# Kernel tuning notes

Hardware: AMD Instinct MI355X
Metric: run time of the kernel (lower is better)

## Reference

```python
import jax, jax.numpy as jnp
import numpy as np
import math

# Dimensions (see shape_source)
B, C, NH = 4, 256, 8
VP, VW = 6, 16   # vertical: patches-per-window (outer), windows (inner)
HP, HW = 32, 3   # horizontal: patches-per-window (outer), windows (inner)
NW, P = VW * HW, VP * HP   # 48 windows, 192 patches per window
GRID = 96                   # patch grid is 96x96
SHIFT = (HP // 2, VP // 2)  # (16, 3) = (window_shape[0]//2, window_shape[1]//2)
FF = 4 * C
SCALE = 1.0 / math.sqrt(C)  # source divides by sqrt(embedding_dim), not head_dim


def setup_inputs() -> dict:
    key = jax.random.key(0)
    ks = jax.random.split(key, 17)
    std = 0.02
    n = lambda k, s: (jax.random.normal(k, s, dtype=jnp.float32) * std)
    return {
        "embeddings": jax.random.normal(ks[0], (B, GRID, GRID, C), dtype=jnp.float32),
        "ln1_g": jnp.ones((C,), jnp.float32), "ln1_b": jnp.zeros((C,), jnp.float32),
        "wq": n(ks[1], (C, C)), "bq": jnp.zeros((C,), jnp.float32),
        "wk": n(ks[2], (C, C)), "bk": jnp.zeros((C,), jnp.float32),
        "wv": n(ks[3], (C, C)), "bv": jnp.zeros((C,), jnp.float32),
        "pos_bias": n(ks[4], (NH, P, P)),
        "ln2_g": jnp.ones((C,), jnp.float32), "ln2_b": jnp.zeros((C,), jnp.float32),
        "w1": n(ks[5], (C, FF)), "b1": jnp.zeros((FF,), jnp.float32),
        "w2": n(ks[6], (FF, C)), "b2": jnp.zeros((C,), jnp.float32),
    }


def _ln(x, g, b, eps=1e-5):
    m = jnp.mean(x, axis=-1, keepdims=True)
    v = jnp.mean(jnp.square(x - m), axis=-1, keepdims=True)
    return (x - m) * jax.lax.rsqrt(v + eps) * g + b


def reference(embeddings, ln1_g, ln1_b, wq, bq, wk, bk, wv, bv, pos_bias,
              ln2_g, ln2_b, w1, b1, w2, b2):
    x = jnp.roll(embeddings, SHIFT, axis=(1, 2))
    # part: H=(VP outer, VW inner), W=(HP outer, HW inner) -> [B, NW, P, C]
    p = x.reshape(B, VP, VW, HP, HW, C).transpose(0, 2, 4, 1, 3, 5).reshape(B, NW, P, C)
    y = _ln(p, ln1_g, ln1_b)
    def heads(w, b):
        return (y @ w + b).reshape(B, NW, P, NH, C // NH).transpose(0, 1, 3, 2, 4)
    q, k, v = heads(wq, bq), heads(wk, bk), heads(wv, bv)  # [B, NW, NH, P, Dh]
    logits = jnp.einsum('bwhpd,bwhqd->bwhpq', q, k) * SCALE + pos_bias
    attn = jax.nn.softmax(logits, axis=-1)
    sa = jnp.einsum('bwhpq,bwhqd->bwhpd', attn, v)
    sa = sa.transpose(0, 1, 3, 2, 4).reshape(B, NW, P, C)
    a = p + sa
    h = _ln(a, ln2_g, ln2_b)
    ff = jax.nn.gelu(h @ w1 + b1, approximate=False) @ w2 + b2
    out = a + ff
    # join: inverse of part
    o = out.reshape(B, VW, HW, VP, HP, C).transpose(0, 3, 1, 4, 2, 5).reshape(B, GRID, GRID, C)
    return jnp.roll(o, (-SHIFT[0], -SHIFT[1]), axis=(1, 2))
```

## Files before the change

kernel.cpp:

```cpp
#include <hip/hip_runtime.h>
#include <hip/hip_bf16.h>
#include <cstdint>

using bf16x8 = __attribute__((ext_vector_type(8))) short;
using f32x4  = __attribute__((ext_vector_type(4))) float;
using bf16_t = __hip_bfloat16;

#define DEVI static __device__ __forceinline__

constexpr int kB = 4, kC = 256, kNH = 8, kDh = 32;
constexpr int kVP = 6, kVW = 16, kHP = 32, kHW = 3;
constexpr int kNW = 48, kP = 192, kGRID = 96;
constexpr int kRows = kB * kNW * kP;
constexpr int kFF = 1024;
constexpr float kScale = 0.0625f;

DEVI void row_coords(int row, int& b, int& g1, int& g2) {
  int b_  = row / (kNW * kP);
  int rem = row - b_ * (kNW * kP);
  int w = rem / kP;
  int p = rem - w * kP;
  int vw = w / kHW, hw = w - vw * kHW;
  int vp = p >> 5,  hp = p & 31;
  int r  = vp * kVW + vw;
  int cc = hp * kHW + hw;
  g1 = r + 80;  if (g1 >= kGRID) g1 -= kGRID;
  g2 = cc + 93; if (g2 >= kGRID) g2 -= kGRID;
  b = b_;
}

DEVI float bf2f(short s) {
  union { unsigned u; float f; } c;
  c.u = ((unsigned)(unsigned short)s) << 16;
  return c.f;
}
DEVI short f2bf(float f) {
  bf16_t h = __float2bfloat16(f);
  return *reinterpret_cast<short*>(&h);
}

DEVI void gload16(const void* g, void* l) {
  __builtin_amdgcn_global_load_lds(
      (__attribute__((address_space(1))) void*)(uintptr_t)g,
      (__attribute__((address_space(3))) void*)(uintptr_t)l, 16, 0, 0);
}

DEVI bf16x8 ds_read_b128(uint32_t byte_off) {
  bf16x8 v;
  asm volatile("ds_read_b128 %0, %1" : "=v"(v) : "v"(byte_off));
  return v;
}

DEVI float gelu_fast(float v) {
  const float t2 = v * 1.5957691216f * (1.f + 0.044715f * v * v);
  return v / (1.f + __expf(fminf(-t2, 60.f)));
}

__global__ __launch_bounds__(256) void k_wconv(
    const float* __restrict__ wq, const float* __restrict__ wk,
    const float* __restrict__ wv, const float* __restrict__ w1,
    const float* __restrict__ w2, bf16_t* __restrict__ W) {
  const int i = blockIdx.x * 256 + threadIdx.x;
  if (i < 196608) {
    const int n = i >> 8, k = i & 255;
    const float* src = n < 256 ? wq : (n < 512 ? wk : wv);
    W[i] = __float2bfloat16(src[k * 256 + (n & 255)]);
  } else if (i < 458752) {
    const int j = i - 196608;
    const int n = j >> 8, k = j & 255;
    W[i] = __float2bfloat16(w1[k * 1024 + n]);
  } else if (i < 720896) {
    const int j = i - 458752;
    const int n = j >> 10, k = j & 1023;
    W[i] = __float2bfloat16(w2[k * 256 + n]);
  }
}

__global__ __launch_bounds__(256) void k_ln1(const float* __restrict__ emb,
    const float* __restrict__ gam, const float* __restrict__ bet,
    bf16_t* __restrict__ Y) {
  const int wave = threadIdx.x >> 6, lane = threadIdx.x & 63;
  #pragma unroll
  for (int rr = 0; rr < 2; ++rr) {
    const int row = blockIdx.x * 8 + wave * 2 + rr;
    int b, g1, g2; row_coords(row, b, g1, g2);
    const float* src = emb + (((size_t)b * kGRID + g1) * kGRID + g2) * kC;
    float4 x = *reinterpret_cast<const float4*>(src + lane * 4);
    float s  = x.x + x.y + x.z + x.w;
    float sq = x.x*x.x + x.y*x.y + x.z*x.z + x.w*x.w;
    #pragma unroll
    for (int off = 32; off; off >>= 1) { s += __shfl_xor(s, off); sq += __shfl_xor(sq, off); }
    const float mean = s * (1.f / kC);
    const float rstd = rsqrtf(sq * (1.f / kC) - mean * mean + 1e-5f);
    const float4 g4 = *reinterpret_cast<const float4*>(gam + lane * 4);
    const float4 b4 = *reinterpret_cast<const float4*>(bet + lane * 4);
    short4 o;
    o.x = f2bf((x.x - mean) * rstd * g4.x + b4.x);
    o.y = f2bf((x.y - mean) * rstd * g4.y + b4.y);
    o.z = f2bf((x.z - mean) * rstd * g4.z + b4.z);
    o.w = f2bf((x.w - mean) * rstd * g4.w + b4.w);
    *reinterpret_cast<short4*>(Y + (size_t)row * kC + lane * 4) = o;
  }
}

__global__ __launch_bounds__(256) void k_ln2(const float* __restrict__ emb,
    const bf16_t* __restrict__ SA,
    const float* __restrict__ gam, const float* __restrict__ bet,
    float* __restrict__ A, bf16_t* __restrict__ H) {
  const int wave = threadIdx.x >> 6, lane = threadIdx.x & 63;
  #pragma unroll
  for (int rr = 0; rr < 2; ++rr) {
    const int row = blockIdx.x * 8 + wave * 2 + rr;
    int b, g1, g2; row_coords(row, b, g1, g2);
    const float* src = emb + (((size_t)b * kGRID + g1) * kGRID + g2) * kC;
    float4 x = *reinterpret_cast<const float4*>(src + lane * 4);
    short4 sv = *reinterpret_cast<const short4*>(SA + (size_t)row * kC + lane * 4);
    x.x += bf2f(sv.x); x.y += bf2f(sv.y); x.z += bf2f(sv.z); x.w += bf2f(sv.w);
    *reinterpret_cast<float4*>(A + (size_t)row * kC + lane * 4) = x;
    float s  = x.x + x.y + x.z + x.w;
    float sq = x.x*x.x + x.y*x.y + x.z*x.z + x.w*x.w;
    #pragma unroll
    for (int off = 32; off; off >>= 1) { s += __shfl_xor(s, off); sq += __shfl_xor(sq, off); }
    const float mean = s * (1.f / kC);
    const float rstd = rsqrtf(sq * (1.f / kC) - mean * mean + 1e-5f);
    const float4 g4 = *reinterpret_cast<const float4*>(gam + lane * 4);
    const float4 b4 = *reinterpret_cast<const float4*>(bet + lane * 4);
    short4 o;
    o.x = f2bf((x.x - mean) * rstd * g4.x + b4.x);
    o.y = f2bf((x.y - mean) * rstd * g4.y + b4.y);
    o.z = f2bf((x.z - mean) * rstd * g4.z + b4.z);
    o.w = f2bf((x.w - mean) * rstd * g4.w + b4.w);
    *reinterpret_cast<short4*>(H + (size_t)row * kC + lane * 4) = o;
  }
}

template <int KDIM, int EPI, int GX>
__global__ __launch_bounds__(256, 4) void k_gemm6(
    const bf16_t* __restrict__ Amat, const bf16_t* __restrict__ BT,
    const float* __restrict__ bias0, const float* __restrict__ bias1,
    const float* __restrict__ bias2,
    bf16_t* __restrict__ Obf, const float* __restrict__ Ares,
    float* __restrict__ Out) {
  __shared__ short sm[16384];
  bf16_t* const As0 = (bf16_t*)&sm[0];
  bf16_t* const As1 = (bf16_t*)&sm[4096];
  bf16_t* const Bs0 = (bf16_t*)&sm[8192];
  bf16_t* const Bs1 = (bf16_t*)&sm[12288];
  const int tid = threadIdx.x;
  const int wave = tid >> 6, lane = tid & 63;
  const int lr = lane & 15, kg4 = lane >> 4;
  const int nwg = (kRows / 128) * GX;
  const int wg = (blockIdx.x & 7) * (nwg >> 3) + (blockIdx.x >> 3);
  const int m0 = (wg / GX) * 128, n0 = (wg % GX) * 128;
  const int wm = (wave >> 1) * 64, wn = (wave & 1) * 64;
  const int srow = lane >> 2;
  const int scol = ((lane & 3) ^ (srow & 3)) << 3;

  auto stage = [&](bf16_t* aDst, bf16_t* bDst, int k0) {
    #pragma unroll
    for (int i = 0; i < 2; ++i) {
      const int c = wave * 2 + i;
      const int row = c * 16 + srow;
      gload16(Amat + (size_t)(m0 + row) * KDIM + k0 + scol, aDst + c * 512);
      gload16(BT   + (size_t)(n0 + row) * KDIM + k0 + scol, bDst + c * 512);
    }
  };

  const uint32_t aOff0 = (uint32_t)(uintptr_t)As0;
  const uint32_t aOff1 = (uint32_t)(uintptr_t)As1;
  const uint32_t bOff0 = (uint32_t)(uintptr_t)Bs0;
  const uint32_t bOff1 = (uint32_t)(uintptr_t)Bs1;

  f32x4 acc[4][4] = {};
  auto compute = [&](uint32_t aBase, uint32_t bBase) {
    bf16x8 af[4], bq[4];
    #pragma unroll
    for (int m = 0; m < 4; ++m) {
      const int r = wm + m * 16 + lr;
      af[m] = ds_read_b128(aBase + r * 64 + ((kg4 ^ (r & 3)) << 4));
    }
    #pragma unroll
    for (int n = 0; n < 4; ++n) {
      const int r = wn + n * 16 + lr;
      bq[n] = ds_read_b128(bBase + r * 64 + ((kg4 ^ (r & 3)) << 4));
    }
    asm volatile("s_waitcnt lgkmcnt(0)" ::: "memory");
    __builtin_amdgcn_sched_barrier(0);
    __builtin_amdgcn_s_setprio(1);
    #pragma unroll
    for (int m = 0; m < 4; ++m)
      #pragma unroll
      for (int n = 0; n < 4; ++n)
        acc[m][n] = __builtin_amdgcn_mfma_f32_16x16x32_bf16(af[m], bq[n], acc[m][n], 0, 0, 0);
    __builtin_amdgcn_s_setprio(0);
  };

  stage(As0, Bs0, 0);
  constexpr int NT = KDIM / 32;
  #pragma unroll
  for (int t = 0; t < NT; ++t) {
    if (t + 1 < NT) {
      stage(((t + 1) & 1) ? As1 : As0, ((t + 1) & 1) ? Bs1 : Bs0, (t + 1) * 32);
      asm volatile("s_waitcnt vmcnt(4)" ::: "memory");
    } else {
      asm volatile("s_waitcnt vmcnt(0)" ::: "memory");
    }
    __builtin_amdgcn_sched_barrier(0);
    __builtin_amdgcn_s_barrier();
    compute((t & 1) ? aOff1 : aOff0, (t & 1) ? bOff1 : bOff0);
    __builtin_amdgcn_s_barrier();
  }
  __builtin_amdgcn_sched_barrier(0);

  if constexpr (EPI == 0 || EPI == 1) {
    short* scr = &sm[wave * 4096];
    const int colbase = n0 + wn;
    const float* bp;
    int cb;
    if constexpr (EPI == 0) {
      const int which = colbase >> 8;
      bp = which == 0 ? bias0 : (which == 1 ? bias1 : bias2);
      cb = colbase & 255;
    } else { bp = bias0; cb = colbase; }
    #pragma unroll
    for (int m = 0; m < 4; ++m)
      #pragma unroll
      for (int n = 0; n < 4; ++n)
        #pragma unroll
        for (int r = 0; r < 4; ++r) {
          const int lrow = m * 16 + kg4 * 4 + r;
          const int lcol = n * 16 + lr;
          float v = acc[m][n][r] + bp[cb + lcol];
          if constexpr (EPI == 1) v = gelu_fast(v);
          const int sc = lcol ^ ((lrow & 3) << 4);
          scr[lrow * 64 + sc] = f2bf(v);
        }
    const int rl = lane >> 3, cl = (lane & 7) * 8;
    bf16_t* const obase = (EPI == 0)
        ? Obf + (size_t)(colbase >> 8) * kRows * kC
        : Obf;
    const int ld = (EPI == 0) ? kC : kFF;
    #pragma unroll
    for (int p = 0; p < 8; ++p) {
      const int lrow = p * 8 + rl;
      const int sc = cl ^ ((lrow & 3) << 4);
      bf16x8 v = *reinterpret_cast<const bf16x8*>(&scr[lrow * 64 + sc]);
      *reinterpret_cast<bf16x8*>(
          obase + (size_t)(m0 + wm + lrow) * ld + cb + cl) = v;
    }
  } else {
    float* scrf = reinterpret_cast<float*>(&sm[wave * 4096]);
    #pragma unroll
    for (int h = 0; h < 2; ++h) {
      #pragma unroll
      for (int m = 0; m < 4; ++m)
        #pragma unroll
        for (int nn = 0; nn < 2; ++nn) {
          const int n = h * 2 + nn;
          #pragma unroll
          for (int r = 0; r < 4; ++r) {
            const int lrow = m * 16 + kg4 * 4 + r;
            const int lcol = nn * 16 + lr;
            scrf[lrow * 32 + (lcol ^ ((lrow & 3) << 3))] =
                acc[m][n][r] + bias0[n0 + wn + n * 16 + lr];
          }
        }
      const int rl = lane >> 3, cl = (lane & 7) * 4;
      #pragma unroll
      for (int p = 0; p < 8; ++p) {
        const int lrow = p * 8 + rl;
        const int row = m0 + wm + lrow;
        const int col = n0 + wn + h * 32 + cl;
        float4 v = *reinterpret_cast<const float4*>(
            &scrf[lrow * 32 + (cl ^ ((lrow & 3) << 3))]);
        const float4 a4 = *reinterpret_cast<const float4*>(
            &Ares[(size_t)row * kC + col]);
        v.x += a4.x; v.y += a4.y; v.z += a4.z; v.w += a4.w;
        int b, g1, g2; row_coords(row, b, g1, g2);
        *reinterpret_cast<float4*>(
            &Out[(((size_t)b * kGRID + g1) * kGRID + g2) * kC + col]) = v;
      }
      if (h == 0) __builtin_amdgcn_s_barrier();
    }
  }
}

constexpr int kKsPad = 40;
constexpr int kVtPad = 200;
constexpr int kPlPad = 200;
__global__ __launch_bounds__(256) void k_attn(
    const bf16_t* __restrict__ Q, const bf16_t* __restrict__ K,
    const bf16_t* __restrict__ V, const float* __restrict__ pos,
    bf16_t* __restrict__ SA) {
  __shared__ short Ks[kP * kKsPad];
  __shared__ short Vt[kDh * kVtPad];
  __shared__ short Pl[4 * 16 * kPlPad];
  const int bw = blockIdx.x >> 3, h = blockIdx.x & 7;
  const int rowbase = bw * kP, colbase = h * kDh;
  const int tid = threadIdx.x, wave = tid >> 6, lane = tid & 63;
  const int lr = lane & 15, kg = lane >> 4;
  const int wq0 = wave * 48;
  const float* pb = pos + (size_t)h * kP * kP;

  #pragma unroll
  for (int i = 0; i < 3; ++i) {
    const int c = tid + i * 256;
    const int row = c >> 2, dch = (c & 3) * 8;
    const size_t gbase = (size_t)(rowbase + row) * kC + colbase + dch;
    bf16x8 kv = *reinterpret_cast<const bf16x8*>(K + gbase);
    *reinterpret_cast<bf16x8*>(&Ks[row * kKsPad + dch]) = kv;
    bf16x8 vv = *reinterpret_cast<const bf16x8*>(V + gbase);
    #pragma unroll
    for (int e = 0; e < 8; ++e) Vt[(dch + e) * kVtPad + row] = vv[e];
  }
  __syncthreads();

  for (int m = 0; m < 3; ++m) {
    const int rbase = wq0 + m * 16;
    bf16x8 aq = *reinterpret_cast<const bf16x8*>(
        Q + (size_t)(rowbase + rbase + lr) * kC + colbase + kg * 8);
    f32x4 s[12];
    #pragma unroll
    for (int n = 0; n < 12; ++n) {
      bf16x8 bk = *reinterpret_cast<const bf16x8*>(&Ks[(n * 16 + lr) * kKsPad + kg * 8]);
      s[n] = __builtin_amdgcn_mfma_f32_16x16x32_bf16(aq, bk, (f32x4){0.f, 0.f, 0.f, 0.f}, 0, 0, 0);
    }
    float mx[4] = {-1e30f, -1e30f, -1e30f, -1e30f};
    #pragma unroll
    for (int n = 0; n < 12; ++n) {
      #pragma unroll
      for (int r = 0; r < 4; ++r) {
        const float lg = fmaf(s[n][r], kScale,
                              pb[(size_t)(rbase + kg * 4 + r) * kP + n * 16 + lr]);
        s[n][r] = lg;
        mx[r] = fmaxf(mx[r], lg);
      }
    }
    #pragma unroll
    for (int r = 0; r < 4; ++r)
      #pragma unroll
      for (int off = 8; off; off >>= 1) mx[r] = fmaxf(mx[r], __shfl_xor(mx[r], off));
    float sm4[4] = {0.f, 0.f, 0.f, 0.f};
    #pragma unroll
    for (int n = 0; n < 12; ++n)
      #pragma unroll
      for (int r = 0; r < 4; ++r) {
        const float e = __expf(s[n][r] - mx[r]);
        s[n][r] = e;
        sm4[r] += e;
      }
    #pragma unroll
    for (int r = 0; r < 4; ++r) {
      #pragma unroll
      for (int off = 8; off; off >>= 1) sm4[r] += __shfl_xor(sm4[r], off);
      sm4[r] = 1.f / sm4[r];
    }
    #pragma unroll
    for (int n = 0; n < 12; ++n)
      #pragma unroll
      for (int r = 0; r < 4; ++r)
        Pl[(wave * 16 + kg * 4 + r) * kPlPad + n * 16 + lr] = f2bf(s[n][r] * sm4[r]);
    f32x4 o0 = {0.f, 0.f, 0.f, 0.f}, o1 = {0.f, 0.f, 0.f, 0.f};
    #pragma unroll
    for (int kk = 0; kk < 6; ++kk) {
      bf16x8 ap = *reinterpret_cast<const bf16x8*>(&Pl[(wave * 16 + lr) * kPlPad + kk * 32 + kg * 8]);
      bf16x8 b0 = *reinterpret_cast<const bf16x8*>(&Vt[lr * kVtPad + kk * 32 + kg * 8]);
      bf16x8 b1 = *reinterpret_cast<const bf16x8*>(&Vt[(16 + lr) * kVtPad + kk * 32 + kg * 8]);
      o0 = __builtin_amdgcn_mfma_f32_16x16x32_bf16(ap, b0, o0, 0, 0, 0);
      o1 = __builtin_amdgcn_mfma_f32_16x16x32_bf16(ap, b1, o1, 0, 0, 0);
    }
    short* scr2 = &Pl[wave * 16 * kPlPad];
    #pragma unroll
    for (int r = 0; r < 4; ++r) {
      scr2[(kg * 4 + r) * 32 + lr]      = f2bf(o0[r]);
      scr2[(kg * 4 + r) * 32 + 16 + lr] = f2bf(o1[r]);
    }
    {
      const int rrow = lane >> 2, c0 = (lane & 3) * 8;
      bf16x8 v = *reinterpret_cast<const bf16x8*>(&scr2[rrow * 32 + c0]);
      *reinterpret_cast<bf16x8*>(
          SA + (size_t)(rowbase + rbase + rrow) * kC + colbase + c0) = v;
    }
  }
}

extern "C" void kernel_launch(void* const* d_in, const int* in_sizes, int n_in,
                              void* d_out, int out_size, void* d_ws, size_t ws_size,
                              hipStream_t stream) {
  const float* emb  = (const float*)d_in[0];
  const float* ln1g = (const float*)d_in[1];
  const float* ln1b = (const float*)d_in[2];
  const float* wq   = (const float*)d_in[3];
  const float* bq   = (const float*)d_in[4];
  const float* wk   = (const float*)d_in[5];
  const float* bk   = (const float*)d_in[6];
  const float* wv   = (const float*)d_in[7];
  const float* bv   = (const float*)d_in[8];
  const float* pos  = (const float*)d_in[9];
  const float* ln2g = (const float*)d_in[10];
  const float* ln2b = (const float*)d_in[11];
  const float* w1   = (const float*)d_in[12];
  const float* b1   = (const float*)d_in[13];
  const float* w2   = (const float*)d_in[14];
  const float* b2   = (const float*)d_in[15];

  char* ws = (char*)d_ws;
  const size_t nYb = (size_t)kRows * kC * 2;
  bf16_t* Y    = (bf16_t*)(ws);
  bf16_t* Qb   = (bf16_t*)(ws + nYb);
  bf16_t* SAb  = (bf16_t*)(ws + nYb * 4);
  float*  Abuf = (float*) (ws + nYb * 5);
  bf16_t* H    = (bf16_t*)(ws + nYb * 5 + (size_t)kRows * kC * 4);
  bf16_t* G    = (bf16_t*)(ws);
  bf16_t* W    = (bf16_t*)(ws + nYb * 5 + (size_t)kRows * kC * 4 + nYb);
  bf16_t* WqkvT = W;
  bf16_t* W1T   = W + 768 * 256;
  bf16_t* W2T   = W1T + 1024 * 256;

  k_wconv<<<2816, 256, 0, stream>>>(wq, wk, wv, w1, w2, W);
  k_ln1<<<kRows / 8, 256, 0, stream>>>(emb, ln1g, ln1b, Y);
  k_gemm6<256, 0, 6><<<(kRows / 128) * 6, 256, 0, stream>>>(
      Y, WqkvT, bq, bk, bv, Qb, nullptr, nullptr);
  k_attn<<<kB * kNW * kNH, 256, 0, stream>>>(
      Qb, Qb + (size_t)kRows * kC, Qb + 2 * (size_t)kRows * kC, pos, SAb);
  k_ln2<<<kRows / 8, 256, 0, stream>>>(emb, SAb, ln2g, ln2b, Abuf, H);
  k_gemm6<256, 1, 8><<<(kRows / 128) * 8, 256, 0, stream>>>(
      H, W1T, b1, nullptr, nullptr, G, nullptr, nullptr);
  k_gemm6<1024, 2, 2><<<(kRows / 128) * 2, 256, 0, stream>>>(
      G, W2T, b2, nullptr, nullptr, nullptr, Abuf, (float*)d_out);
}
```

Before: 177.3 us.

## Enlarge GEMM tiles to 256x256 with 512-thread workgroups

Replaces the 128x128, 4-wave GEMM with a 256x256 tile computed by 8 waves. Each wave now owns a 128x64 sub-tile, and the LDS double buffers are doubled in size. The aim is more operand reuse per global load and fewer workgroups. The epilogues are restructured to drain the larger accumulator through per-wave scratch in chunks, with a new swizzle. The cost is far fewer blocks: only 144 for the FFN down-projection, which may leave many CUs idle and cut latency hiding at one workgroup per CU.

```diff
diff --git a/kernel.cpp b/kernel.cpp
--- a/kernel.cpp
+++ b/kernel.cpp
@@ -135,24 +135,24 @@
 }
 
 template <int KDIM, int EPI, int GX>
-__global__ __launch_bounds__(256, 4) void k_gemm6(
+__global__ __launch_bounds__(512, 1) void k_gemm7(
     const bf16_t* __restrict__ Amat, const bf16_t* __restrict__ BT,
     const float* __restrict__ bias0, const float* __restrict__ bias1,
     const float* __restrict__ bias2,
     bf16_t* __restrict__ Obf, const float* __restrict__ Ares,
     float* __restrict__ Out) {
-  __shared__ short sm[16384];
+  __shared__ short sm[32768];
   bf16_t* const As0 = (bf16_t*)&sm[0];
-  bf16_t* const As1 = (bf16_t*)&sm[4096];
-  bf16_t* const Bs0 = (bf16_t*)&sm[8192];
-  bf16_t* const Bs1 = (bf16_t*)&sm[12288];
+  bf16_t* const As1 = (bf16_t*)&sm[8192];
+  bf16_t* const Bs0 = (bf16_t*)&sm[16384];
+  bf16_t* const Bs1 = (bf16_t*)&sm[24576];
   const int tid = threadIdx.x;
   const int wave = tid >> 6, lane = tid & 63;
   const int lr = lane & 15, kg4 = lane >> 4;
-  const int nwg = (kRows / 128) * GX;
+  const int nwg = (kRows / 256) * GX;
   const int wg = (blockIdx.x & 7) * (nwg >> 3) + (blockIdx.x >> 3);
-  const int m0 = (wg / GX) * 128, n0 = (wg % GX) * 128;
-  const int wm = (wave >> 1) * 64, wn = (wave & 1) * 64;
+  const int m0 = (wg / GX) * 256, n0 = (wg % GX) * 256;
+  const int wm = (wave >> 2) * 128, wn = (wave & 3) * 64;
   const int srow = lane >> 2;
   const int scol = ((lane & 3) ^ (srow & 3)) << 3;
 
@@ -171,11 +171,11 @@
   const uint32_t bOff0 = (uint32_t)(uintptr_t)Bs0;
   const uint32_t bOff1 = (uint32_t)(uintptr_t)Bs1;
 
-  f32x4 acc[4][4] = {};
+  f32x4 acc[8][4] = {};
   auto compute = [&](uint32_t aBase, uint32_t bBase) {
-    bf16x8 af[4], bq[4];
-    #pragma unroll
-    for (int m = 0; m < 4; ++m) {
+    bf16x8 af[8], bq[4];
+    #pragma unroll
+    for (int m = 0; m < 8; ++m) {
       const int r = wm + m * 16 + lr;
       af[m] = ds_read_b128(aBase + r * 64 + ((kg4 ^ (r & 3)) << 4));
     }
@@ -188,7 +188,7 @@
     __builtin_amdgcn_sched_barrier(0);
     __builtin_amdgcn_s_setprio(1);
     #pragma unroll
-    for (int m = 0; m < 4; ++m)
+    for (int m = 0; m < 8; ++m)
       #pragma unroll
       for (int n = 0; n < 4; ++n)
         acc[m][n] = __builtin_amdgcn_mfma_f32_16x16x32_bf16(af[m], bq[n], acc[m][n], 0, 0, 0);
@@ -222,65 +222,71 @@
       bp = which == 0 ? bias0 : (which == 1 ? bias1 : bias2);
       cb = colbase & 255;
     } else { bp = bias0; cb = colbase; }
-    #pragma unroll
-    for (int m = 0; m < 4; ++m)
-      #pragma unroll
-      for (int n = 0; n < 4; ++n)
-        #pragma unroll
-        for (int r = 0; r < 4; ++r) {
-          const int lrow = m * 16 + kg4 * 4 + r;
-          const int lcol = n * 16 + lr;
-          float v = acc[m][n][r] + bp[cb + lcol];
-          if constexpr (EPI == 1) v = gelu_fast(v);
-          const int sc = lcol ^ ((lrow & 3) << 4);
-          scr[lrow * 64 + sc] = f2bf(v);
-        }
-    const int rl = lane >> 3, cl = (lane & 7) * 8;
     bf16_t* const obase = (EPI == 0)
-        ? Obf + (size_t)(colbase >> 8) * kRows * kC
+        ? Obf + (size_t)((n0 + wn) >> 8) * kRows * kC
         : Obf;
     const int ld = (EPI == 0) ? kC : kFF;
-    #pragma unroll
-    for (int p = 0; p < 8; ++p) {
-      const int lrow = p * 8 + rl;
-      const int sc = cl ^ ((lrow & 3) << 4);
-      bf16x8 v = *reinterpret_cast<const bf16x8*>(&scr[lrow * 64 + sc]);
-      *reinterpret_cast<bf16x8*>(
-          obase + (size_t)(m0 + wm + lrow) * ld + cb + cl) = v;
+    const int rl = lane >> 3, cl = (lane & 7) * 8;
+    #pragma unroll
+    for (int h = 0; h < 2; ++h) {
+      #pragma unroll
+      for (int mm = 0; mm < 4; ++mm) {
+        const int m = h * 4 + mm;
+        #pragma unroll
+        for (int n = 0; n < 4; ++n)
+          #pragma unroll
+          for (int r = 0; r < 4; ++r) {
+            const int lrow = mm * 16 + kg4 * 4 + r;
+            const int lcol = n * 16 + lr;
+            float v = acc[m][n][r] + bp[cb + lcol];
+            if constexpr (EPI == 1) v = gelu_fast(v);
+            scr[lrow * 64 + (lcol ^ (((lrow >> 2) & 3) << 4))] = f2bf(v);
+          }
+      }
+      #pragma unroll
+      for (int p = 0; p < 8; ++p) {
+        const int lrow = p * 8 + rl;
+        bf16x8 v = *reinterpret_cast<const bf16x8*>(
+            &scr[lrow * 64 + (cl ^ (((lrow >> 2) & 3) << 4))]);
+        *reinterpret_cast<bf16x8*>(
+            obase + (size_t)(m0 + wm + h * 64 + lrow) * ld + cb + cl) = v;
+      }
     }
   } else {
     float* scrf = reinterpret_cast<float*>(&sm[wave * 4096]);
-    #pragma unroll
-    for (int h = 0; h < 2; ++h) {
-      #pragma unroll
-      for (int m = 0; m < 4; ++m)
+    const int rl = lane >> 3, cl = (lane & 7) * 4;
+    #pragma unroll
+    for (int q = 0; q < 4; ++q) {
+      #pragma unroll
+      for (int mm = 0; mm < 2; ++mm) {
+        const int m = q * 2 + mm;
         #pragma unroll
-        for (int nn = 0; nn < 2; ++nn) {
-          const int n = h * 2 + nn;
+        for (int n = 0; n < 4; ++n)
           #pragma unroll
           for (int r = 0; r < 4; ++r) {
-            const int lrow = m * 16 + kg4 * 4 + r;
-            const int lcol = nn * 16 + lr;
-            scrf[lrow * 32 + (lcol ^ ((lrow & 3) << 3))] =
-                acc[m][n][r] + bias0[n0 + wn + n * 16 + lr];
+            const int lrow = mm * 16 + kg4 * 4 + r;
+            const int lcol = n * 16 + lr;
+            scrf[lrow * 64 + (lcol ^ (((lrow >> 2) & 3) << 4))] =
+                acc[m][n][r] + bias0[n0 + wn + lcol];
           }
+      }
+      #pragma unroll
+      for (int p = 0; p < 4; ++p)
+        #pragma unroll
+        for (int ch = 0; ch < 2; ++ch) {
+          const int lrow = p * 8 + rl;
+          const int lcol = ch * 32 + cl;
+          float4 v = *reinterpret_cast<const float4*>(
+              &scrf[lrow * 64 + (lcol ^ (((lrow >> 2) & 3) << 4))]);
+          const int row = m0 + wm + q * 32 + lrow;
+          const int col = n0 + wn + lcol;
+          const float4 a4 = *reinterpret_cast<const float4*>(
+              &Ares[(size_t)row * kC + col]);
+          v.x += a4.x; v.y += a4.y; v.z += a4.z; v.w += a4.w;
+          int b, g1, g2; row_coords(row, b, g1, g2);
+          *reinterpret_cast<float4*>(
+              &Out[(((size_t)b * kGRID + g1) * kGRID + g2) * kC + col]) = v;
         }
-      const int rl = lane >> 3, cl = (lane & 7) * 4;
-      #pragma unroll
-      for (int p = 0; p < 8; ++p) {
-        const int lrow = p * 8 + rl;
-        const int row = m0 + wm + lrow;
-        const int col = n0 + wn + h * 32 + cl;
-        float4 v = *reinterpret_cast<const float4*>(
-            &scrf[lrow * 32 + (cl ^ ((lrow & 3) << 3))]);
-        const float4 a4 = *reinterpret_cast<const float4*>(
-            &Ares[(size_t)row * kC + col]);
-        v.x += a4.x; v.y += a4.y; v.z += a4.z; v.w += a4.w;
-        int b, g1, g2; row_coords(row, b, g1, g2);
-        *reinterpret_cast<float4*>(
-            &Out[(((size_t)b * kGRID + g1) * kGRID + g2) * kC + col]) = v;
-      }
-      if (h == 0) __builtin_amdgcn_s_barrier();
     }
   }
 }
@@ -419,13 +425,13 @@
 
   k_wconv<<<2816, 256, 0, stream>>>(wq, wk, wv, w1, w2, W);
   k_ln1<<<kRows / 8, 256, 0, stream>>>(emb, ln1g, ln1b, Y);
-  k_gemm6<256, 0, 6><<<(kRows / 128) * 6, 256, 0, stream>>>(
+  k_gemm7<256, 0, 3><<<(kRows / 256) * 3, 512, 0, stream>>>(
       Y, WqkvT, bq, bk, bv, Qb, nullptr, nullptr);
   k_attn<<<kB * kNW * kNH, 256, 0, stream>>>(
       Qb, Qb + (size_t)kRows * kC, Qb + 2 * (size_t)kRows * kC, pos, SAb);
   k_ln2<<<kRows / 8, 256, 0, stream>>>(emb, SAb, ln2g, ln2b, Abuf, H);
-  k_gemm6<256, 1, 8><<<(kRows / 128) * 8, 256, 0, stream>>>(
+  k_gemm7<256, 1, 4><<<(kRows / 256) * 4, 512, 0, stream>>>(
       H, W1T, b1, nullptr, nullptr, G, nullptr, nullptr);
-  k_gemm6<1024, 2, 2><<<(kRows / 128) * 2, 256, 0, stream>>>(
+  k_gemm7<1024, 2, 1><<<(kRows / 256) * 1, 512, 0, stream>>>(
       G, W2T, b2, nullptr, nullptr, nullptr, Abuf, (float*)d_out);
 }
```

After: 207.4 us. +17.0%, slower.

## Triple-buffer GEMM LDS stages and change swizzle to reduce bank conflicts

Applied to the files above, without the earlier changes.

The GEMM kernel moves from a double-buffered LDS pipeline to three buffers with a prefetch distance of two k-tiles, which removes the second barrier per iteration. The XOR swizzle changes from row bits 0-1 to row bits 1-2 (and 2-3 in the epilogue scratch) to cut LDS bank conflicts. The larger shared-memory footprint lowers the occupancy hint from 4 to 3 blocks per CU, and the single-barrier ordering depends on correct vmcnt accounting for in-flight loads.

```diff
diff --git a/kernel.cpp b/kernel.cpp
--- a/kernel.cpp
+++ b/kernel.cpp
@@ -135,17 +135,15 @@
 }
 
 template <int KDIM, int EPI, int GX>
-__global__ __launch_bounds__(256, 4) void k_gemm6(
+__global__ __launch_bounds__(256, 3) void k_gemm8(
     const bf16_t* __restrict__ Amat, const bf16_t* __restrict__ BT,
     const float* __restrict__ bias0, const float* __restrict__ bias1,
     const float* __restrict__ bias2,
     bf16_t* __restrict__ Obf, const float* __restrict__ Ares,
     float* __restrict__ Out) {
-  __shared__ short sm[16384];
-  bf16_t* const As0 = (bf16_t*)&sm[0];
-  bf16_t* const As1 = (bf16_t*)&sm[4096];
-  bf16_t* const Bs0 = (bf16_t*)&sm[8192];
-  bf16_t* const Bs1 = (bf16_t*)&sm[12288];
+  __shared__ short sm[24576];
+  bf16_t* As[3] = {(bf16_t*)&sm[0], (bf16_t*)&sm[4096], (bf16_t*)&sm[8192]};
+  bf16_t* Bs[3] = {(bf16_t*)&sm[12288], (bf16_t*)&sm[16384], (bf16_t*)&sm[20480]};
   const int tid = threadIdx.x;
   const int wave = tid >> 6, lane = tid & 63;
   const int lr = lane & 15, kg4 = lane >> 4;
@@ -154,7 +152,7 @@
   const int m0 = (wg / GX) * 128, n0 = (wg % GX) * 128;
   const int wm = (wave >> 1) * 64, wn = (wave & 1) * 64;
   const int srow = lane >> 2;
-  const int scol = ((lane & 3) ^ (srow & 3)) << 3;
+  const int scol = ((lane & 3) ^ ((srow >> 1) & 3)) << 3;
 
   auto stage = [&](bf16_t* aDst, bf16_t* bDst, int k0) {
     #pragma unroll
@@ -166,10 +164,10 @@
     }
   };
 
-  const uint32_t aOff0 = (uint32_t)(uintptr_t)As0;
-  const uint32_t aOff1 = (uint32_t)(uintptr_t)As1;
-  const uint32_t bOff0 = (uint32_t)(uintptr_t)Bs0;
-  const uint32_t bOff1 = (uint32_t)(uintptr_t)Bs1;
+  const uint32_t aOff[3] = {(uint32_t)(uintptr_t)As[0], (uint32_t)(uintptr_t)As[1],
+                            (uint32_t)(uintptr_t)As[2]};
+  const uint32_t bOff[3] = {(uint32_t)(uintptr_t)Bs[0], (uint32_t)(uintptr_t)Bs[1],
+                            (uint32_t)(uintptr_t)Bs[2]};
 
   f32x4 acc[4][4] = {};
   auto compute = [&](uint32_t aBase, uint32_t bBase) {
@@ -177,12 +175,12 @@
     #pragma unroll
     for (int m = 0; m < 4; ++m) {
       const int r = wm + m * 16 + lr;
-      af[m] = ds_read_b128(aBase + r * 64 + ((kg4 ^ (r & 3)) << 4));
+      af[m] = ds_read_b128(aBase + r * 64 + ((kg4 ^ ((r >> 1) & 3)) << 4));
     }
     #pragma unroll
     for (int n = 0; n < 4; ++n) {
       const int r = wn + n * 16 + lr;
-      bq[n] = ds_read_b128(bBase + r * 64 + ((kg4 ^ (r & 3)) << 4));
+      bq[n] = ds_read_b128(bBase + r * 64 + ((kg4 ^ ((r >> 1) & 3)) << 4));
     }
     asm volatile("s_waitcnt lgkmcnt(0)" ::: "memory");
     __builtin_amdgcn_sched_barrier(0);
@@ -195,21 +193,23 @@
     __builtin_amdgcn_s_setprio(0);
   };
 
-  stage(As0, Bs0, 0);
+  stage(As[0], Bs[0], 0);
+  if (KDIM > 32) stage(As[1], Bs[1], 32);
   constexpr int NT = KDIM / 32;
   #pragma unroll
   for (int t = 0; t < NT; ++t) {
     if (t + 1 < NT) {
-      stage(((t + 1) & 1) ? As1 : As0, ((t + 1) & 1) ? Bs1 : Bs0, (t + 1) * 32);
       asm volatile("s_waitcnt vmcnt(4)" ::: "memory");
     } else {
       asm volatile("s_waitcnt vmcnt(0)" ::: "memory");
     }
     __builtin_amdgcn_sched_barrier(0);
     __builtin_amdgcn_s_barrier();
-    compute((t & 1) ? aOff1 : aOff0, (t & 1) ? bOff1 : bOff0);
-    __builtin_amdgcn_s_barrier();
-  }
+    if (t + 2 < NT)
+      stage(As[(t + 2) % 3], Bs[(t + 2) % 3], (t + 2) * 32);
+    compute(aOff[t % 3], bOff[t % 3]);
+  }
+  __builtin_amdgcn_s_barrier();
   __builtin_amdgcn_sched_barrier(0);
 
   if constexpr (EPI == 0 || EPI == 1) {
@@ -232,8 +232,7 @@
           const int lcol = n * 16 + lr;
           float v = acc[m][n][r] + bp[cb + lcol];
           if constexpr (EPI == 1) v = gelu_fast(v);
-          const int sc = lcol ^ ((lrow & 3) << 4);
-          scr[lrow * 64 + sc] = f2bf(v);
+          scr[lrow * 64 + (lcol ^ (((lrow >> 2) & 3) << 4))] = f2bf(v);
         }
     const int rl = lane >> 3, cl = (lane & 7) * 8;
     bf16_t* const obase = (EPI == 0)
@@ -243,8 +242,8 @@
     #pragma unroll
     for (int p = 0; p < 8; ++p) {
       const int lrow = p * 8 + rl;
-      const int sc = cl ^ ((lrow & 3) << 4);
-      bf16x8 v = *reinterpret_cast<const bf16x8*>(&scr[lrow * 64 + sc]);
+      bf16x8 v = *reinterpret_cast<const bf16x8*>(
+          &scr[lrow * 64 + (cl ^ (((lrow >> 2) & 3) << 4))]);
       *reinterpret_cast<bf16x8*>(
           obase + (size_t)(m0 + wm + lrow) * ld + cb + cl) = v;
     }
@@ -261,7 +260,7 @@
           for (int r = 0; r < 4; ++r) {
             const int lrow = m * 16 + kg4 * 4 + r;
             const int lcol = nn * 16 + lr;
-            scrf[lrow * 32 + (lcol ^ ((lrow & 3) << 3))] =
+            scrf[lrow * 32 + (lcol ^ (((lrow >> 2) & 3) << 3))] =
                 acc[m][n][r] + bias0[n0 + wn + n * 16 + lr];
           }
         }
@@ -272,7 +271,7 @@
         const int row = m0 + wm + lrow;
         const int col = n0 + wn + h * 32 + cl;
         float4 v = *reinterpret_cast<const float4*>(
-            &scrf[lrow * 32 + (cl ^ ((lrow & 3) << 3))]);
+            &scrf[lrow * 32 + (cl ^ (((lrow >> 2) & 3) << 3))]);
         const float4 a4 = *reinterpret_cast<const float4*>(
             &Ares[(size_t)row * kC + col]);
         v.x += a4.x; v.y += a4.y; v.z += a4.z; v.w += a4.w;
@@ -419,13 +418,13 @@
 
   k_wconv<<<2816, 256, 0, stream>>>(wq, wk, wv, w1, w2, W);
   k_ln1<<<kRows / 8, 256, 0, stream>>>(emb, ln1g, ln1b, Y);
-  k_gemm6<256, 0, 6><<<(kRows / 128) * 6, 256, 0, stream>>>(
+  k_gemm8<256, 0, 6><<<(kRows / 128) * 6, 256, 0, stream>>>(
       Y, WqkvT, bq, bk, bv, Qb, nullptr, nullptr);
   k_attn<<<kB * kNW * kNH, 256, 0, stream>>>(
       Qb, Qb + (size_t)kRows * kC, Qb + 2 * (size_t)kRows * kC, pos, SAb);
   k_ln2<<<kRows / 8, 256, 0, stream>>>(emb, SAb, ln2g, ln2b, Abuf, H);
-  k_gemm6<256, 1, 8><<<(kRows / 128) * 8, 256, 0, stream>>>(
+  k_gemm8<256, 1, 8><<<(kRows / 128) * 8, 256, 0, stream>>>(
       H, W1T, b1, nullptr, nullptr, G, nullptr, nullptr);
-  k_gemm6<1024, 2, 2><<<(kRows / 128) * 2, 256, 0, stream>>>(
+  k_gemm8<1024, 2, 2><<<(kRows / 128) * 2, 256, 0, stream>>>(
       G, W2T, b2, nullptr, nullptr, nullptr, Abuf, (float*)d_out);
 }
```

Measured after the change: 176.5 us. About the same (-0.4%).
